# Kernel tuning notes

Hardware: AMD Instinct MI355X
Metric: run time of the kernel (lower is better)

Reference implementation:

```python
import jax, jax.numpy as jnp
import numpy as np

B, N, DIM = 16, 4096, 256
EXP = 4
COV_EPS = 1e-08


def setup_inputs() -> dict:
    key = jax.random.key(0)
    ks = jax.random.split(key, 9)
    s = 1.0 / np.sqrt(DIM)
    sh = 1.0 / np.sqrt(DIM * EXP)
    return {
        "x": jax.random.normal(ks[0], (B, N, DIM), dtype=jnp.float32),
        # IsoFFN: Linear(dim, 4*dim) -> GELU -> Linear(4*dim, dim) + residual (dropout inactive at eval)
        "W1": jax.random.uniform(ks[1], (DIM, DIM * EXP), minval=-s, maxval=s, dtype=jnp.float32),
        "b1": jnp.zeros((DIM * EXP,), jnp.float32),
        "W2": jax.random.uniform(ks[2], (DIM * EXP, DIM), minval=-sh, maxval=sh, dtype=jnp.float32),
        "b2": jnp.zeros((DIM,), jnp.float32),
        # eigenvalue head: Linear(dim, 3) + Softplus
        "Wval": jax.random.uniform(ks[3], (DIM, 3), minval=-s, maxval=s, dtype=jnp.float32),
        "bval": jnp.zeros((3,), jnp.float32),
        # eigenvector head: Linear(dim, 9)
        "Wvec": jax.random.uniform(ks[4], (DIM, 9), minval=-s, maxval=s, dtype=jnp.float32),
        "bvec": jnp.zeros((9,), jnp.float32),
    }


def reference(x, W1, b1, W2, b2, Wval, bval, Wvec, bvec):
    b, n, c = x.shape
    # IsoFFN (eval mode: dropout = identity), residual connection
    h = x + jax.nn.gelu(x @ W1 + b1) @ W2 + b2
    # eigenvalue head -> positive eigenvalues -> diagonal [B*N, 3, 3]
    eigvals = jax.nn.softplus(h @ Wval + bval).reshape(b * n, 3)
    L = jnp.zeros((b * n, 3, 3), h.dtype).at[:, jnp.arange(3), jnp.arange(3)].set(eigvals)
    # eigenvector head -> batched tiny QR to orthonormalize
    V = (h @ Wvec + bvec).reshape(b * n, 3, 3)
    Q, _ = jnp.linalg.qr(V)  # batched 3x3 QR
    # cov = Q L Q^T
    cov = jnp.einsum('bij,bjk,blk->bil', Q, L, Q).reshape(b, n, 3, 3)
    cov = (cov + jnp.swapaxes(cov, -2, -1)) * 0.5
    cov = cov + COV_EPS * jnp.eye(3, dtype=cov.dtype)
    return cov
```

## Files before the change

kernel.cpp:

```cpp
#include <hip/hip_runtime.h>
#include <cstdint>
#include <cstddef>

#define TOKENS   65536
#define KDIM     256
#define HIDDEN   1024
#define BM       128
#define HC       32
#define NCHUNK   32
#define NTHREADS 512
#define NBLOCKS  (TOKENS / BM)

#define W2OFF  32768
#define GOFF   65536
#define ACCOFF 81920
#define B1OFF  98304
#define LDS_BYTES 131072

using f16x8 = __attribute__((ext_vector_type(8))) _Float16;
using f16x4 = __attribute__((ext_vector_type(4))) _Float16;
using f32x4 = __attribute__((ext_vector_type(4))) float;
using u32x4 = __attribute__((ext_vector_type(4))) uint32_t;

__device__ __align__(16) _Float16 g_W1h[NCHUNK * HC * KDIM];
__device__ __align__(16) _Float16 g_W1l[NCHUNK * HC * KDIM];
__device__ __align__(16) _Float16 g_W2h[NCHUNK * KDIM * HC];
__device__ __align__(16) _Float16 g_W2l[NCHUNK * KDIM * HC];
__device__ __align__(16) _Float16 g_Whh[16 * KDIM];
__device__ __align__(16) _Float16 g_Whl[16 * KDIM];

__global__ __launch_bounds__(256) void prep_kernel(
    const float* __restrict__ W1, const float* __restrict__ W2,
    const float* __restrict__ Wval, const float* __restrict__ Wvec) {
  const int tid = blockIdx.x * 256 + threadIdx.x;
  if (tid < 32768) {
    const int c = tid >> 10, n = (tid >> 5) & 31, gd = tid & 31;
    const int g = gd ^ (n & 7);
    const int hid = c * 32 + n;
    f16x8 hv, lv;
#pragma unroll
    for (int j = 0; j < 8; ++j) {
      const float wv = W1[(g * 8 + j) * HIDDEN + hid];
      const _Float16 hi = (_Float16)wv;
      hv[j] = hi;
      lv[j] = (_Float16)(wv - (float)hi);
    }
    const int dst = c * 8192 + n * 256 + gd * 8;
    *(f16x8*)(g_W1h + dst) = hv;
    *(f16x8*)(g_W1l + dst) = lv;
  } else if (tid < 65536) {
    const int t = tid - 32768;
    const int c = t >> 10, n = (t >> 2) & 255, gd = t & 3;
    const int g = gd ^ ((n >> 1) & 3);
    f16x8 hv, lv;
#pragma unroll
    for (int j = 0; j < 8; ++j) {
      const float wv = W2[(c * 32 + g * 8 + j) * KDIM + n];
      const _Float16 hi = (_Float16)wv;
      hv[j] = hi;
      lv[j] = (_Float16)(wv - (float)hi);
    }
    const int dst = c * 8192 + n * 32 + gd * 8;
    *(f16x8*)(g_W2h + dst) = hv;
    *(f16x8*)(g_W2l + dst) = lv;
  } else if (tid < 65536 + 4096) {
    const int e = tid - 65536;
    const int j16 = e >> 8, k = e & 255;
    float wv = 0.f;
    if (j16 < 3) wv = Wval[k * 3 + j16];
    else if (j16 < 12) wv = Wvec[k * 9 + (j16 - 3)];
    const _Float16 hi = (_Float16)wv;
    g_Whh[e] = hi;
    g_Whl[e] = (_Float16)(wv - (float)hi);
  }
}

__device__ __forceinline__ void stage_W1(char* smem, int c, int w, int lane) {
  const char* base = (w < 4) ? (const char*)g_W1h : (const char*)g_W1l;
  const char* s = base + (size_t)c * 16384 + (size_t)(w & 3) * 4096 + (size_t)lane * 16;
  char* d = smem + ((w < 4) ? 0 : 16384) + (w & 3) * 4096;
#pragma unroll
  for (int i = 0; i < 4; ++i) {
    __builtin_amdgcn_global_load_lds(
        (__attribute__((address_space(1))) void*)(void*)(s + i * 1024),
        (__attribute__((address_space(3))) void*)(d + i * 1024), 16, 0, 0);
  }
}
__device__ __forceinline__ void stage_W2(char* smem, int c, int w, int lane) {
  const char* base = (w < 4) ? (const char*)g_W2h : (const char*)g_W2l;
  const char* s = base + (size_t)c * 16384 + (size_t)(w & 3) * 4096 + (size_t)lane * 16;
  char* d = smem + W2OFF + ((w < 4) ? 0 : 16384) + (w & 3) * 4096;
#pragma unroll
  for (int i = 0; i < 4; ++i) {
    __builtin_amdgcn_global_load_lds(
        (__attribute__((address_space(1))) void*)(void*)(s + i * 1024),
        (__attribute__((address_space(3))) void*)(d + i * 1024), 16, 0, 0);
  }
}

__device__ __forceinline__ f16x8 unpack_half(const u32x4 a, const u32x4 b, uint32_t sel) {
  u32x4 r;
  r[0] = __builtin_amdgcn_perm(a[1], a[0], sel);
  r[1] = __builtin_amdgcn_perm(a[3], a[2], sel);
  r[2] = __builtin_amdgcn_perm(b[1], b[0], sel);
  r[3] = __builtin_amdgcn_perm(b[3], b[2], sel);
  return __builtin_bit_cast(f16x8, r);
}

#define MFMA16(a, b, c) __builtin_amdgcn_mfma_f32_16x16x32_f16((a), (b), (c), 0, 0, 0)

__global__ __launch_bounds__(NTHREADS, 2) void fused_kernel(
    const float* __restrict__ x, const float* __restrict__ b1,
    const float* __restrict__ b2, const float* __restrict__ bval,
    const float* __restrict__ bvec, float* __restrict__ out) {
  extern __shared__ char smem[];
  const int tid  = threadIdx.x;
  const int lane = tid & 63;
  const int w    = tid >> 6;
  const int wm   = w & 3;
  const int wp   = w >> 2;
  const int l15  = lane & 15;
  const int lg   = lane >> 4;
  const int64_t R = (int64_t)blockIdx.x * BM;

  {
    const float* xg = x + R * KDIM;
#pragma unroll
    for (int i = 0; i < 16; ++i) {
      const int fidx = tid + NTHREADS * i;
      const int row  = fidx >> 6;
      const int f4   = fidx & 63;
      const float4 v = *(const float4*)(xg + row * KDIM + f4 * 4);
      const _Float16 h0 = (_Float16)v.x, h1 = (_Float16)v.y,
                     h2 = (_Float16)v.z, h3 = (_Float16)v.w;
      f16x4 hv = {h0, h1, h2, h3};
      f16x4 lv = {(_Float16)(v.x - (float)h0), (_Float16)(v.y - (float)h1),
                  (_Float16)(v.z - (float)h2), (_Float16)(v.w - (float)h3)};
      const uint32_t off = (uint32_t)(row * 512) +
                           (((uint32_t)(f4 * 8)) ^ ((row & 7) << 4));
      *(f16x4*)(smem + off)         = hv;
      *(f16x4*)(smem + 65536 + off) = lv;
    }
  }
  __syncthreads();

  f16x8 xa[2][8];
  {
    const char* xplane = smem + wp * 65536;
#pragma unroll
    for (int mt = 0; mt < 2; ++mt) {
      const int row = wm * 32 + mt * 16 + l15;
      const uint32_t rbase = row * 512;
      const uint32_t swz = (row & 7) << 4;
#pragma unroll
      for (int ks = 0; ks < 8; ++ks) {
        const uint32_t off = rbase + (((uint32_t)((ks * 32 + lg * 8) * 2)) ^ swz);
        xa[mt][ks] = *(const f16x8*)(xplane + off);
      }
    }
  }
  __syncthreads();

  {
    float* b1l = (float*)(smem + B1OFF);
    b1l[tid]       = b1[tid];
    b1l[tid + 512] = b1[tid + 512];
  }
  stage_W1(smem, 0, w, lane);
  __syncthreads();

  const f32x4 z4 = {0.f, 0.f, 0.f, 0.f};
  f32x4 acc2[2][8];
#pragma unroll
  for (int mt = 0; mt < 2; ++mt)
#pragma unroll
    for (int nt = 0; nt < 8; ++nt) acc2[mt][nt] = z4;

#pragma unroll 1
  for (int t = 0; t < NCHUNK; ++t) {
    stage_W2(smem, t, w, lane);

    f32x4 accG[8] = {z4, z4, z4, z4, z4, z4, z4, z4};
    {
      const uint32_t swz   = (uint32_t)((l15 & 7) << 4);
      const uint32_t base0 = (uint32_t)(l15 * 512);
      const uint32_t base1 = (uint32_t)((16 + l15) * 512);
      if (wp == 0) {
#pragma unroll
        for (int ks = 0; ks < 8; ++ks) {
          const uint32_t off = ((uint32_t)(ks * 64 + lg * 16)) ^ swz;
          const f16x8 bh0 = *(const f16x8*)(smem + base0 + off);
          const f16x8 bh1 = *(const f16x8*)(smem + base1 + off);
          const f16x8 bl0 = *(const f16x8*)(smem + 16384 + base0 + off);
          const f16x8 bl1 = *(const f16x8*)(smem + 16384 + base1 + off);
          accG[0] = MFMA16(xa[0][ks], bh0, accG[0]);
          accG[1] = MFMA16(xa[1][ks], bh0, accG[1]);
          accG[2] = MFMA16(xa[0][ks], bh1, accG[2]);
          accG[3] = MFMA16(xa[1][ks], bh1, accG[3]);
          accG[4] = MFMA16(xa[0][ks], bl0, accG[4]);
          accG[5] = MFMA16(xa[1][ks], bl0, accG[5]);
          accG[6] = MFMA16(xa[0][ks], bl1, accG[6]);
          accG[7] = MFMA16(xa[1][ks], bl1, accG[7]);
        }
      } else {
#pragma unroll
        for (int ks = 0; ks < 8; ++ks) {
          const uint32_t off = ((uint32_t)(ks * 64 + lg * 16)) ^ swz;
          const f16x8 bh0 = *(const f16x8*)(smem + base0 + off);
          const f16x8 bh1 = *(const f16x8*)(smem + base1 + off);
          accG[0] = MFMA16(xa[0][ks], bh0, accG[0]);
          accG[1] = MFMA16(xa[1][ks], bh0, accG[1]);
          accG[2] = MFMA16(xa[0][ks], bh1, accG[2]);
          accG[3] = MFMA16(xa[1][ks], bh1, accG[3]);
        }
#pragma unroll
        for (int nt = 0; nt < 2; ++nt) {
#pragma unroll
          for (int mt = 0; mt < 2; ++mt) {
#pragma unroll
            for (int r = 0; r < 4; ++r) {
              const int row = wm * 32 + mt * 16 + lg * 4 + r;
              const int col = nt * 16 + l15;
              const uint32_t off = (uint32_t)(ACCOFF + row * 128) +
                                   (((uint32_t)(col * 4)) ^ ((row & 7) << 4));
              *(float*)(smem + off) = accG[nt * 2 + mt][r];
            }
          }
        }
      }
    }
    asm volatile("s_waitcnt lgkmcnt(0)" ::: "memory");
    __builtin_amdgcn_s_barrier();
    __builtin_amdgcn_sched_barrier(0);

    if (t < NCHUNK - 1) stage_W1(smem, t + 1, w, lane);

    if (wp == 0) {
      constexpr float C2 = -1.5957691216057308f;
      constexpr float A2 = -0.071355071222456f;
#pragma unroll
      for (int nt = 0; nt < 2; ++nt) {
        const float bv = ((const float*)(smem + B1OFF))[t * 32 + nt * 16 + l15];
#pragma unroll
        for (int mt = 0; mt < 2; ++mt) {
#pragma unroll
          for (int r = 0; r < 4; ++r) {
            const int row = wm * 32 + mt * 16 + lg * 4 + r;
            const int col = nt * 16 + l15;
            const uint32_t soff = (((uint32_t)(col * 4)) ^ ((row & 7) << 4));
            const float c = *(const float*)(smem + ACCOFF + row * 128 + soff);
            const float v  = accG[nt * 2 + mt][r] + accG[4 + nt * 2 + mt][r] + c + bv;
            const float v2 = v * v;
            const float tE = v * __builtin_fmaf(v2, A2, C2);
            const float e  = __expf(tE);
            const float gv = __fdividef(v, 1.f + e);
            const _Float16 gh = (_Float16)gv;
            const _Float16 gl = (_Float16)(gv - (float)gh);
            const uint32_t pk = (uint32_t)__builtin_bit_cast(unsigned short, gh) |
                                ((uint32_t)__builtin_bit_cast(unsigned short, gl) << 16);
            *(uint32_t*)(smem + GOFF + row * 128 + soff) = pk;
          }
        }
      }
    }
    asm volatile("s_waitcnt lgkmcnt(0)" ::: "memory");
    if (t == NCHUNK - 1) { asm volatile("s_waitcnt vmcnt(0)" ::: "memory"); }
    else                 { asm volatile("s_waitcnt vmcnt(4)" ::: "memory"); }
    __builtin_amdgcn_s_barrier();
    __builtin_amdgcn_sched_barrier(0);

    {
      f16x8 ah[2], al[2];
#pragma unroll
      for (int mt = 0; mt < 2; ++mt) {
        const int row = wm * 32 + mt * 16 + l15;
        const uint32_t sw = (uint32_t)((row & 7) << 4);
        const uint32_t base = (uint32_t)(GOFF + row * 128);
        const u32x4 w0 = *(const u32x4*)(smem + base + (((uint32_t)(lg * 32)) ^ sw));
        const u32x4 w1v = *(const u32x4*)(smem + base + (((uint32_t)(lg * 32 + 16)) ^ sw));
        ah[mt] = unpack_half(w0, w1v, 0x05040100u);
        al[mt] = unpack_half(w0, w1v, 0x07060302u);
      }
#pragma unroll
      for (int nt = 0; nt < 8; ++nt) {
        const int n = wp * 128 + nt * 16 + l15;
        const uint32_t off = (uint32_t)(n * 64) +
                             (((uint32_t)(lg * 16)) ^ (((n >> 1) & 3) << 4));
        const f16x8 bh = *(const f16x8*)(smem + W2OFF + off);
        const f16x8 bl = *(const f16x8*)(smem + W2OFF + 16384 + off);
#pragma unroll
        for (int mt = 0; mt < 2; ++mt) {
          acc2[mt][nt] = MFMA16(ah[mt], bh, acc2[mt][nt]);
          acc2[mt][nt] = MFMA16(ah[mt], bl, acc2[mt][nt]);
          acc2[mt][nt] = MFMA16(al[mt], bh, acc2[mt][nt]);
        }
      }
    }
    asm volatile("s_waitcnt lgkmcnt(0)" ::: "memory");
    asm volatile("s_waitcnt vmcnt(0)" ::: "memory");
    __builtin_amdgcn_s_barrier();
    __builtin_amdgcn_sched_barrier(0);
  }
  __syncthreads();

  {
    const float* xg = x + R * KDIM;
#pragma unroll
    for (int nt = 0; nt < 8; ++nt) {
      const float bv = b2[wp * 128 + nt * 16 + l15];
#pragma unroll
      for (int mt = 0; mt < 2; ++mt) {
#pragma unroll
        for (int r = 0; r < 4; ++r) {
          const int row = wm * 32 + mt * 16 + lg * 4 + r;
          const int col = wp * 128 + nt * 16 + l15;
          const float h = acc2[mt][nt][r] + xg[row * KDIM + col] + bv;
          acc2[mt][nt][r] = h;
          const uint32_t off = (uint32_t)(row * 512) +
                               (((uint32_t)(col * 2)) ^ ((row & 7) << 4));
          *(_Float16*)(smem + off) = (_Float16)h;
        }
      }
    }
  }
  __syncthreads();

  f32x4 hacc = z4;
  const int hrow = wm * 32 + wp * 16 + l15;
  const uint32_t hbase = hrow * 512;
  const uint32_t hswz  = (hrow & 7) << 4;
#pragma unroll
  for (int ks = 0; ks < 8; ++ks) {
    const uint32_t off = hbase + (((uint32_t)((ks * 32 + lg * 8) * 2)) ^ hswz);
    const f16x8 af  = *(const f16x8*)(smem + off);
    const f16x8 bhf = *(const f16x8*)(g_Whh + l15 * 256 + ks * 32 + lg * 8);
    const f16x8 blf = *(const f16x8*)(g_Whl + l15 * 256 + ks * 32 + lg * 8);
    hacc = MFMA16(af, bhf, hacc);
    hacc = MFMA16(af, blf, hacc);
  }
  __syncthreads();

#pragma unroll
  for (int nt = 0; nt < 8; ++nt) {
#pragma unroll
    for (int mt = 0; mt < 2; ++mt) {
#pragma unroll
      for (int r = 0; r < 4; ++r) {
        const int row = wm * 32 + mt * 16 + lg * 4 + r;
        const int col = wp * 128 + nt * 16 + l15;
        const float h = acc2[mt][nt][r];
        const _Float16 hh = (_Float16)h;
        const uint32_t off = (uint32_t)(row * 512) +
                             (((uint32_t)(col * 2)) ^ ((row & 7) << 4));
        *(_Float16*)(smem + off) = (_Float16)(h - (float)hh);
      }
    }
  }
  __syncthreads();

#pragma unroll
  for (int ks = 0; ks < 8; ++ks) {
    const uint32_t off = hbase + (((uint32_t)((ks * 32 + lg * 8) * 2)) ^ hswz);
    const f16x8 af  = *(const f16x8*)(smem + off);
    const f16x8 bhf = *(const f16x8*)(g_Whh + l15 * 256 + ks * 32 + lg * 8);
    hacc = MFMA16(af, bhf, hacc);
  }
  const float hb = (l15 < 3) ? bval[l15] : ((l15 < 12) ? bvec[l15 - 3] : 0.f);
#pragma unroll
  for (int r = 0; r < 4; ++r) hacc[r] += hb;

  float* hstg = (float*)(smem + 65536);
#pragma unroll
  for (int r = 0; r < 4; ++r) {
    const int row = wm * 32 + wp * 16 + lg * 4 + r;
    hstg[row * 16 + l15] = hacc[r];
  }
  if (lane < 16) {
    const int row = wm * 32 + wp * 16 + lane;
    const float* hs = hstg + row * 16;
    float sp[3];
#pragma unroll
    for (int i = 0; i < 3; ++i) {
      const float s = hs[i];
      sp[i] = fmaxf(s, 0.f) + log1pf(__expf(-fabsf(s)));
    }
    const float a0 = hs[3], a1 = hs[6], a2 = hs[9];
    const float b0 = hs[4], bc1 = hs[7], bc2 = hs[10];
    const float na = a0 * a0 + a1 * a1 + a2 * a2;
    const float ia = 1.f / sqrtf(fmaxf(na, 1e-30f));
    const float q00 = a0 * ia, q01 = a1 * ia, q02 = a2 * ia;
    const float d  = q00 * b0 + q01 * bc1 + q02 * bc2;
    const float u0 = b0 - d * q00, u1 = bc1 - d * q01, u2 = bc2 - d * q02;
    const float nu = u0 * u0 + u1 * u1 + u2 * u2;
    const float iu = 1.f / sqrtf(fmaxf(nu, 1e-30f));
    const float q10 = u0 * iu, q11 = u1 * iu, q12 = u2 * iu;
    const float q20 = q01 * q12 - q02 * q11;
    const float q21 = q02 * q10 - q00 * q12;
    const float q22 = q00 * q11 - q01 * q10;
    const float c00 = sp[0]*q00*q00 + sp[1]*q10*q10 + sp[2]*q20*q20 + 1e-8f;
    const float c11 = sp[0]*q01*q01 + sp[1]*q11*q11 + sp[2]*q21*q21 + 1e-8f;
    const float c22 = sp[0]*q02*q02 + sp[1]*q12*q12 + sp[2]*q22*q22 + 1e-8f;
    const float c01 = sp[0]*q00*q01 + sp[1]*q10*q11 + sp[2]*q20*q21;
    const float c02 = sp[0]*q00*q02 + sp[1]*q10*q12 + sp[2]*q20*q22;
    const float c12 = sp[0]*q01*q02 + sp[1]*q11*q12 + sp[2]*q21*q22;
    float* o = out + (size_t)(R + row) * 9;
    o[0] = c00; o[1] = c01; o[2] = c02;
    o[3] = c01; o[4] = c11; o[5] = c12;
    o[6] = c02; o[7] = c12; o[8] = c22;
  }
}

extern "C" void kernel_launch(void* const* d_in, const int* in_sizes, int n_in,
                              void* d_out, int out_size, void* d_ws, size_t ws_size,
                              hipStream_t stream) {
  const float* x    = (const float*)d_in[0];
  const float* W1   = (const float*)d_in[1];
  const float* b1   = (const float*)d_in[2];
  const float* W2   = (const float*)d_in[3];
  const float* b2   = (const float*)d_in[4];
  const float* Wval = (const float*)d_in[5];
  const float* bval = (const float*)d_in[6];
  const float* Wvec = (const float*)d_in[7];
  const float* bvec = (const float*)d_in[8];
  float* out = (float*)d_out;
  (void)in_sizes; (void)n_in; (void)out_size; (void)d_ws; (void)ws_size;

  hipFuncSetAttribute((const void*)fused_kernel,
                      hipFuncAttributeMaxDynamicSharedMemorySize, LDS_BYTES);

  prep_kernel<<<272, 256, 0, stream>>>(W1, W2, Wval, Wvec);
  fused_kernel<<<NBLOCKS, NTHREADS, LDS_BYTES, stream>>>(x, b1, b2, bval, bvec, out);
}
```

Before: 319.5 us.

## Halve token tile to 64 rows and raise occupancy to four blocks per CU

Shrinks the per-block token tile from 128 to 64 rows, cutting per-wave accumulators and x fragments in half and shrinking LDS so four 512-thread blocks can fit per CU instead of two. The cross-plane partial accumulator exchange for the GELU input is now stored as fp16 instead of fp32. The head epilogue is restricted to the first four waves since only 64 rows remain. In exchange, each W1/W2 chunk staged into LDS is reused across half as many tokens, doubling weight traffic per token. The fp16 partial sum also loses some precision.

```diff
diff --git a/kernel.cpp b/kernel.cpp
--- a/kernel.cpp
+++ b/kernel.cpp
@@ -5,7 +5,7 @@
 #define TOKENS   65536
 #define KDIM     256
 #define HIDDEN   1024
-#define BM       128
+#define BM       64
 #define HC       32
 #define NCHUNK   32
 #define NTHREADS 512
@@ -13,9 +13,9 @@
 
 #define W2OFF  32768
 #define GOFF   65536
-#define ACCOFF 81920
-#define B1OFF  98304
-#define LDS_BYTES 131072
+#define ACCOFF 73728
+#define B1OFF  77824
+#define LDS_BYTES 81920
 
 using f16x8 = __attribute__((ext_vector_type(8))) _Float16;
 using f16x4 = __attribute__((ext_vector_type(4))) _Float16;
@@ -109,7 +109,7 @@
 
 #define MFMA16(a, b, c) __builtin_amdgcn_mfma_f32_16x16x32_f16((a), (b), (c), 0, 0, 0)
 
-__global__ __launch_bounds__(NTHREADS, 2) void fused_kernel(
+__global__ __launch_bounds__(NTHREADS, 4) void fused_kernel(
     const float* __restrict__ x, const float* __restrict__ b1,
     const float* __restrict__ b2, const float* __restrict__ bval,
     const float* __restrict__ bvec, float* __restrict__ out) {
@@ -126,7 +126,7 @@
   {
     const float* xg = x + R * KDIM;
 #pragma unroll
-    for (int i = 0; i < 16; ++i) {
+    for (int i = 0; i < 8; ++i) {
       const int fidx = tid + NTHREADS * i;
       const int row  = fidx >> 6;
       const int f4   = fidx & 63;
@@ -139,24 +139,21 @@
       const uint32_t off = (uint32_t)(row * 512) +
                            (((uint32_t)(f4 * 8)) ^ ((row & 7) << 4));
       *(f16x4*)(smem + off)         = hv;
-      *(f16x4*)(smem + 65536 + off) = lv;
-    }
-  }
-  __syncthreads();
-
-  f16x8 xa[2][8];
+      *(f16x4*)(smem + 32768 + off) = lv;
+    }
+  }
+  __syncthreads();
+
+  f16x8 xa[8];
   {
-    const char* xplane = smem + wp * 65536;
-#pragma unroll
-    for (int mt = 0; mt < 2; ++mt) {
-      const int row = wm * 32 + mt * 16 + l15;
-      const uint32_t rbase = row * 512;
-      const uint32_t swz = (row & 7) << 4;
-#pragma unroll
-      for (int ks = 0; ks < 8; ++ks) {
-        const uint32_t off = rbase + (((uint32_t)((ks * 32 + lg * 8) * 2)) ^ swz);
-        xa[mt][ks] = *(const f16x8*)(xplane + off);
-      }
+    const char* xplane = smem + wp * 32768;
+    const int row = wm * 16 + l15;
+    const uint32_t rbase = row * 512;
+    const uint32_t swz = (row & 7) << 4;
+#pragma unroll
+    for (int ks = 0; ks < 8; ++ks) {
+      const uint32_t off = rbase + (((uint32_t)((ks * 32 + lg * 8) * 2)) ^ swz);
+      xa[ks] = *(const f16x8*)(xplane + off);
     }
   }
   __syncthreads();
@@ -170,17 +167,15 @@
   __syncthreads();
 
   const f32x4 z4 = {0.f, 0.f, 0.f, 0.f};
-  f32x4 acc2[2][8];
-#pragma unroll
-  for (int mt = 0; mt < 2; ++mt)
-#pragma unroll
-    for (int nt = 0; nt < 8; ++nt) acc2[mt][nt] = z4;
+  f32x4 acc2[8];
+#pragma unroll
+  for (int nt = 0; nt < 8; ++nt) acc2[nt] = z4;
 
 #pragma unroll 1
   for (int t = 0; t < NCHUNK; ++t) {
     stage_W2(smem, t, w, lane);
 
-    f32x4 accG[8] = {z4, z4, z4, z4, z4, z4, z4, z4};
+    f32x4 accA[2] = {z4, z4}, accB[2] = {z4, z4};
     {
       const uint32_t swz   = (uint32_t)((l15 & 7) << 4);
       const uint32_t base0 = (uint32_t)(l15 * 512);
@@ -193,14 +188,10 @@
           const f16x8 bh1 = *(const f16x8*)(smem + base1 + off);
           const f16x8 bl0 = *(const f16x8*)(smem + 16384 + base0 + off);
           const f16x8 bl1 = *(const f16x8*)(smem + 16384 + base1 + off);
-          accG[0] = MFMA16(xa[0][ks], bh0, accG[0]);
-          accG[1] = MFMA16(xa[1][ks], bh0, accG[1]);
-          accG[2] = MFMA16(xa[0][ks], bh1, accG[2]);
-          accG[3] = MFMA16(xa[1][ks], bh1, accG[3]);
-          accG[4] = MFMA16(xa[0][ks], bl0, accG[4]);
-          accG[5] = MFMA16(xa[1][ks], bl0, accG[5]);
-          accG[6] = MFMA16(xa[0][ks], bl1, accG[6]);
-          accG[7] = MFMA16(xa[1][ks], bl1, accG[7]);
+          accA[0] = MFMA16(xa[ks], bh0, accA[0]);
+          accA[1] = MFMA16(xa[ks], bh1, accA[1]);
+          accB[0] = MFMA16(xa[ks], bl0, accB[0]);
+          accB[1] = MFMA16(xa[ks], bl1, accB[1]);
         }
       } else {
 #pragma unroll
@@ -208,23 +199,18 @@
           const uint32_t off = ((uint32_t)(ks * 64 + lg * 16)) ^ swz;
           const f16x8 bh0 = *(const f16x8*)(smem + base0 + off);
           const f16x8 bh1 = *(const f16x8*)(smem + base1 + off);
-          accG[0] = MFMA16(xa[0][ks], bh0, accG[0]);
-          accG[1] = MFMA16(xa[1][ks], bh0, accG[1]);
-          accG[2] = MFMA16(xa[0][ks], bh1, accG[2]);
-          accG[3] = MFMA16(xa[1][ks], bh1, accG[3]);
+          accA[0] = MFMA16(xa[ks], bh0, accA[0]);
+          accA[1] = MFMA16(xa[ks], bh1, accA[1]);
         }
 #pragma unroll
         for (int nt = 0; nt < 2; ++nt) {
 #pragma unroll
-          for (int mt = 0; mt < 2; ++mt) {
-#pragma unroll
-            for (int r = 0; r < 4; ++r) {
-              const int row = wm * 32 + mt * 16 + lg * 4 + r;
-              const int col = nt * 16 + l15;
-              const uint32_t off = (uint32_t)(ACCOFF + row * 128) +
-                                   (((uint32_t)(col * 4)) ^ ((row & 7) << 4));
-              *(float*)(smem + off) = accG[nt * 2 + mt][r];
-            }
+          for (int r = 0; r < 4; ++r) {
+            const int row = wm * 16 + lg * 4 + r;
+            const int col = nt * 16 + l15;
+            const uint32_t off = (uint32_t)(ACCOFF + row * 64) +
+                                 (((uint32_t)(col * 2)) ^ ((row & 3) << 4));
+            *(_Float16*)(smem + off) = (_Float16)accA[nt][r];
           }
         }
       }
@@ -242,24 +228,24 @@
       for (int nt = 0; nt < 2; ++nt) {
         const float bv = ((const float*)(smem + B1OFF))[t * 32 + nt * 16 + l15];
 #pragma unroll
-        for (int mt = 0; mt < 2; ++mt) {
-#pragma unroll
-          for (int r = 0; r < 4; ++r) {
-            const int row = wm * 32 + mt * 16 + lg * 4 + r;
-            const int col = nt * 16 + l15;
-            const uint32_t soff = (((uint32_t)(col * 4)) ^ ((row & 7) << 4));
-            const float c = *(const float*)(smem + ACCOFF + row * 128 + soff);
-            const float v  = accG[nt * 2 + mt][r] + accG[4 + nt * 2 + mt][r] + c + bv;
-            const float v2 = v * v;
-            const float tE = v * __builtin_fmaf(v2, A2, C2);
-            const float e  = __expf(tE);
-            const float gv = __fdividef(v, 1.f + e);
-            const _Float16 gh = (_Float16)gv;
-            const _Float16 gl = (_Float16)(gv - (float)gh);
-            const uint32_t pk = (uint32_t)__builtin_bit_cast(unsigned short, gh) |
-                                ((uint32_t)__builtin_bit_cast(unsigned short, gl) << 16);
-            *(uint32_t*)(smem + GOFF + row * 128 + soff) = pk;
-          }
+        for (int r = 0; r < 4; ++r) {
+          const int row = wm * 16 + lg * 4 + r;
+          const int col = nt * 16 + l15;
+          const uint32_t coff = (uint32_t)(ACCOFF + row * 64) +
+                                (((uint32_t)(col * 2)) ^ ((row & 3) << 4));
+          const float c = (float)(*(const _Float16*)(smem + coff));
+          const float v  = accA[nt][r] + accB[nt][r] + c + bv;
+          const float v2 = v * v;
+          const float tE = v * __builtin_fmaf(v2, A2, C2);
+          const float e  = __expf(tE);
+          const float gv = __fdividef(v, 1.f + e);
+          const _Float16 gh = (_Float16)gv;
+          const _Float16 gl = (_Float16)(gv - (float)gh);
+          const uint32_t pk = (uint32_t)__builtin_bit_cast(unsigned short, gh) |
+                              ((uint32_t)__builtin_bit_cast(unsigned short, gl) << 16);
+          const uint32_t goff = (uint32_t)(GOFF + row * 128) +
+                                (((uint32_t)(col * 4)) ^ ((row & 7) << 4));
+          *(uint32_t*)(smem + goff) = pk;
         }
       }
     }
@@ -270,16 +256,15 @@
     __builtin_amdgcn_sched_barrier(0);
 
     {
-      f16x8 ah[2], al[2];
-#pragma unroll
-      for (int mt = 0; mt < 2; ++mt) {
-        const int row = wm * 32 + mt * 16 + l15;
+      f16x8 ah, al;
+      {
+        const int row = wm * 16 + l15;
         const uint32_t sw = (uint32_t)((row & 7) << 4);
         const uint32_t base = (uint32_t)(GOFF + row * 128);
         const u32x4 w0 = *(const u32x4*)(smem + base + (((uint32_t)(lg * 32)) ^ sw));
         const u32x4 w1v = *(const u32x4*)(smem + base + (((uint32_t)(lg * 32 + 16)) ^ sw));
-        ah[mt] = unpack_half(w0, w1v, 0x05040100u);
-        al[mt] = unpack_half(w0, w1v, 0x07060302u);
+        ah = unpack_half(w0, w1v, 0x05040100u);
+        al = unpack_half(w0, w1v, 0x07060302u);
       }
 #pragma unroll
       for (int nt = 0; nt < 8; ++nt) {
@@ -288,12 +273,9 @@
                              (((uint32_t)(lg * 16)) ^ (((n >> 1) & 3) << 4));
         const f16x8 bh = *(const f16x8*)(smem + W2OFF + off);
         const f16x8 bl = *(const f16x8*)(smem + W2OFF + 16384 + off);
-#pragma unroll
-        for (int mt = 0; mt < 2; ++mt) {
-          acc2[mt][nt] = MFMA16(ah[mt], bh, acc2[mt][nt]);
-          acc2[mt][nt] = MFMA16(ah[mt], bl, acc2[mt][nt]);
-          acc2[mt][nt] = MFMA16(al[mt], bh, acc2[mt][nt]);
-        }
+        acc2[nt] = MFMA16(ah, bh, acc2[nt]);
+        acc2[nt] = MFMA16(ah, bl, acc2[nt]);
+        acc2[nt] = MFMA16(al, bh, acc2[nt]);
       }
     }
     asm volatile("s_waitcnt lgkmcnt(0)" ::: "memory");
@@ -309,104 +291,105 @@
     for (int nt = 0; nt < 8; ++nt) {
       const float bv = b2[wp * 128 + nt * 16 + l15];
 #pragma unroll
-      for (int mt = 0; mt < 2; ++mt) {
-#pragma unroll
-        for (int r = 0; r < 4; ++r) {
-          const int row = wm * 32 + mt * 16 + lg * 4 + r;
-          const int col = wp * 128 + nt * 16 + l15;
-          const float h = acc2[mt][nt][r] + xg[row * KDIM + col] + bv;
-          acc2[mt][nt][r] = h;
-          const uint32_t off = (uint32_t)(row * 512) +
-                               (((uint32_t)(col * 2)) ^ ((row & 7) << 4));
-          *(_Float16*)(smem + off) = (_Float16)h;
-        }
+      for (int r = 0; r < 4; ++r) {
+        const int row = wm * 16 + lg * 4 + r;
+        const int col = wp * 128 + nt * 16 + l15;
+        const float h = acc2[nt][r] + xg[row * KDIM + col] + bv;
+        acc2[nt][r] = h;
+        const uint32_t off = (uint32_t)(row * 512) +
+                             (((uint32_t)(col * 2)) ^ ((row & 7) << 4));
+        *(_Float16*)(smem + off) = (_Float16)h;
       }
     }
   }
   __syncthreads();
 
   f32x4 hacc = z4;
-  const int hrow = wm * 32 + wp * 16 + l15;
+  const int hrow = w * 16 + l15;
   const uint32_t hbase = hrow * 512;
   const uint32_t hswz  = (hrow & 7) << 4;
-#pragma unroll
-  for (int ks = 0; ks < 8; ++ks) {
-    const uint32_t off = hbase + (((uint32_t)((ks * 32 + lg * 8) * 2)) ^ hswz);
-    const f16x8 af  = *(const f16x8*)(smem + off);
-    const f16x8 bhf = *(const f16x8*)(g_Whh + l15 * 256 + ks * 32 + lg * 8);
-    const f16x8 blf = *(const f16x8*)(g_Whl + l15 * 256 + ks * 32 + lg * 8);
-    hacc = MFMA16(af, bhf, hacc);
-    hacc = MFMA16(af, blf, hacc);
+  if (w < 4) {
+#pragma unroll
+    for (int ks = 0; ks < 8; ++ks) {
+      const uint32_t off = hbase + (((uint32_t)((ks * 32 + lg * 8) * 2)) ^ hswz);
+      const f16x8 af  = *(const f16x8*)(smem + off);
+      const f16x8 bhf = *(const f16x8*)(g_Whh + l15 * 256 + ks * 32 + lg * 8);
+      const f16x8 blf = *(const f16x8*)(g_Whl + l15 * 256 + ks * 32 + lg * 8);
+      hacc = MFMA16(af, bhf, hacc);
+      hacc = MFMA16(af, blf, hacc);
+    }
   }
   __syncthreads();
 
 #pragma unroll
   for (int nt = 0; nt < 8; ++nt) {
 #pragma unroll
-    for (int mt = 0; mt < 2; ++mt) {
-#pragma unroll
-      for (int r = 0; r < 4; ++r) {
-        const int row = wm * 32 + mt * 16 + lg * 4 + r;
-        const int col = wp * 128 + nt * 16 + l15;
-        const float h = acc2[mt][nt][r];
-        const _Float16 hh = (_Float16)h;
-        const uint32_t off = (uint32_t)(row * 512) +
-                             (((uint32_t)(col * 2)) ^ ((row & 7) << 4));
-        *(_Float16*)(smem + off) = (_Float16)(h - (float)hh);
-      }
-    }
-  }
-  __syncthreads();
-
-#pragma unroll
-  for (int ks = 0; ks < 8; ++ks) {
-    const uint32_t off = hbase + (((uint32_t)((ks * 32 + lg * 8) * 2)) ^ hswz);
-    const f16x8 af  = *(const f16x8*)(smem + off);
-    const f16x8 bhf = *(const f16x8*)(g_Whh + l15 * 256 + ks * 32 + lg * 8);
-    hacc = MFMA16(af, bhf, hacc);
-  }
-  const float hb = (l15 < 3) ? bval[l15] : ((l15 < 12) ? bvec[l15 - 3] : 0.f);
-#pragma unroll
-  for (int r = 0; r < 4; ++r) hacc[r] += hb;
-
-  float* hstg = (float*)(smem + 65536);
-#pragma unroll
-  for (int r = 0; r < 4; ++r) {
-    const int row = wm * 32 + wp * 16 + lg * 4 + r;
-    hstg[row * 16 + l15] = hacc[r];
-  }
-  if (lane < 16) {
-    const int row = wm * 32 + wp * 16 + lane;
-    const float* hs = hstg + row * 16;
-    float sp[3];
-#pragma unroll
-    for (int i = 0; i < 3; ++i) {
-      const float s = hs[i];
-      sp[i] = fmaxf(s, 0.f) + log1pf(__expf(-fabsf(s)));
-    }
-    const float a0 = hs[3], a1 = hs[6], a2 = hs[9];
-    const float b0 = hs[4], bc1 = hs[7], bc2 = hs[10];
-    const float na = a0 * a0 + a1 * a1 + a2 * a2;
-    const float ia = 1.f / sqrtf(fmaxf(na, 1e-30f));
-    const float q00 = a0 * ia, q01 = a1 * ia, q02 = a2 * ia;
-    const float d  = q00 * b0 + q01 * bc1 + q02 * bc2;
-    const float u0 = b0 - d * q00, u1 = bc1 - d * q01, u2 = bc2 - d * q02;
-    const float nu = u0 * u0 + u1 * u1 + u2 * u2;
-    const float iu = 1.f / sqrtf(fmaxf(nu, 1e-30f));
-    const float q10 = u0 * iu, q11 = u1 * iu, q12 = u2 * iu;
-    const float q20 = q01 * q12 - q02 * q11;
-    const float q21 = q02 * q10 - q00 * q12;
-    const float q22 = q00 * q11 - q01 * q10;
-    const float c00 = sp[0]*q00*q00 + sp[1]*q10*q10 + sp[2]*q20*q20 + 1e-8f;
-    const float c11 = sp[0]*q01*q01 + sp[1]*q11*q11 + sp[2]*q21*q21 + 1e-8f;
-    const float c22 = sp[0]*q02*q02 + sp[1]*q12*q12 + sp[2]*q22*q22 + 1e-8f;
-    const float c01 = sp[0]*q00*q01 + sp[1]*q10*q11 + sp[2]*q20*q21;
-    const float c02 = sp[0]*q00*q02 + sp[1]*q10*q12 + sp[2]*q20*q22;
-    const float c12 = sp[0]*q01*q02 + sp[1]*q11*q12 + sp[2]*q21*q22;
-    float* o = out + (size_t)(R + row) * 9;
-    o[0] = c00; o[1] = c01; o[2] = c02;
-    o[3] = c01; o[4] = c11; o[5] = c12;
-    o[6] = c02; o[7] = c12; o[8] = c22;
+    for (int r = 0; r < 4; ++r) {
+      const int row = wm * 16 + lg * 4 + r;
+      const int col = wp * 128 + nt * 16 + l15;
+      const float h = acc2[nt][r];
+      const _Float16 hh = (_Float16)h;
+      const uint32_t off = (uint32_t)(row * 512) +
+                           (((uint32_t)(col * 2)) ^ ((row & 7) << 4));
+      *(_Float16*)(smem + off) = (_Float16)(h - (float)hh);
+    }
+  }
+  __syncthreads();
+
+  if (w < 4) {
+#pragma unroll
+    for (int ks = 0; ks < 8; ++ks) {
+      const uint32_t off = hbase + (((uint32_t)((ks * 32 + lg * 8) * 2)) ^ hswz);
+      const f16x8 af  = *(const f16x8*)(smem + off);
+      const f16x8 bhf = *(const f16x8*)(g_Whh + l15 * 256 + ks * 32 + lg * 8);
+      hacc = MFMA16(af, bhf, hacc);
+    }
+    const float hb = (l15 < 3) ? bval[l15] : ((l15 < 12) ? bvec[l15 - 3] : 0.f);
+#pragma unroll
+    for (int r = 0; r < 4; ++r) hacc[r] += hb;
+  }
+  __syncthreads();
+
+  float* hstg = (float*)(smem + 32768);
+  if (w < 4) {
+#pragma unroll
+    for (int r = 0; r < 4; ++r) {
+      const int row = w * 16 + lg * 4 + r;
+      hstg[row * 16 + l15] = hacc[r];
+    }
+    if (lane < 16) {
+      const int row = w * 16 + lane;
+      const float* hs = hstg + row * 16;
+      float sp[3];
+#pragma unroll
+      for (int i = 0; i < 3; ++i) {
+        const float s = hs[i];
+        sp[i] = fmaxf(s, 0.f) + log1pf(__expf(-fabsf(s)));
+      }
+      const float a0 = hs[3], a1 = hs[6], a2 = hs[9];
+      const float b0 = hs[4], bc1 = hs[7], bc2 = hs[10];
+      const float na = a0 * a0 + a1 * a1 + a2 * a2;
+      const float ia = 1.f / sqrtf(fmaxf(na, 1e-30f));
+      const float q00 = a0 * ia, q01 = a1 * ia, q02 = a2 * ia;
+      const float d  = q00 * b0 + q01 * bc1 + q02 * bc2;
+      const float u0 = b0 - d * q00, u1 = bc1 - d * q01, u2 = bc2 - d * q02;
+      const float nu = u0 * u0 + u1 * u1 + u2 * u2;
+      const float iu = 1.f / sqrtf(fmaxf(nu, 1e-30f));
+      const float q10 = u0 * iu, q11 = u1 * iu, q12 = u2 * iu;
+      const float q20 = q01 * q12 - q02 * q11;
+      const float q21 = q02 * q10 - q00 * q12;
+      const float q22 = q00 * q11 - q01 * q10;
+      const float c00 = sp[0]*q00*q00 + sp[1]*q10*q10 + sp[2]*q20*q20 + 1e-8f;
+      const float c11 = sp[0]*q01*q01 + sp[1]*q11*q11 + sp[2]*q21*q21 + 1e-8f;
+      const float c22 = sp[0]*q02*q02 + sp[1]*q12*q12 + sp[2]*q22*q22 + 1e-8f;
+      const float c01 = sp[0]*q00*q01 + sp[1]*q10*q11 + sp[2]*q20*q21;
+      const float c02 = sp[0]*q00*q02 + sp[1]*q10*q12 + sp[2]*q20*q22;
+      const float c12 = sp[0]*q01*q02 + sp[1]*q11*q12 + sp[2]*q21*q22;
+      float* o = out + (size_t)(R + row) * 9;
+      o[0] = c00; o[1] = c01; o[2] = c02;
+      o[3] = c01; o[4] = c11; o[5] = c12;
+      o[6] = c02; o[7] = c12; o[8] = c22;
+    }
   }
 }
 
```

After: 319.4 us. Within noise of the previous version (-0.1%).

## Double hidden chunk width to 64 and reuse G buffer for partial accumulators

Applied to the files above, without the earlier changes.

Widens each hidden-dimension chunk from 32 to 64 columns, which halves the number of loop iterations and their barriers, and resizes the W1/W2 staging layouts and swizzles to match. The cross-wave partial accumulator now goes through the G region as fp16 in place of a separate fp32 area, and the b1 bias is prefetched into registers instead of being staged in LDS. The cost is more LDS (163840 bytes), which may reduce occupancy below two blocks per CU, plus extra precision loss from storing the partial sum in fp16.

```diff
diff --git a/kernel.cpp b/kernel.cpp
--- a/kernel.cpp
+++ b/kernel.cpp
@@ -6,16 +6,14 @@
 #define KDIM     256
 #define HIDDEN   1024
 #define BM       128
-#define HC       32
-#define NCHUNK   32
+#define HC       64
+#define NCHUNK   16
 #define NTHREADS 512
 #define NBLOCKS  (TOKENS / BM)
 
-#define W2OFF  32768
-#define GOFF   65536
-#define ACCOFF 81920
-#define B1OFF  98304
-#define LDS_BYTES 131072
+#define W2OFF  65536
+#define GOFF   131072
+#define LDS_BYTES 163840
 
 using f16x8 = __attribute__((ext_vector_type(8))) _Float16;
 using f16x4 = __attribute__((ext_vector_type(4))) _Float16;
@@ -34,9 +32,9 @@
     const float* __restrict__ Wval, const float* __restrict__ Wvec) {
   const int tid = blockIdx.x * 256 + threadIdx.x;
   if (tid < 32768) {
-    const int c = tid >> 10, n = (tid >> 5) & 31, gd = tid & 31;
+    const int c = tid >> 11, n = (tid >> 5) & 63, gd = tid & 31;
     const int g = gd ^ (n & 7);
-    const int hid = c * 32 + n;
+    const int hid = c * 64 + n;
     f16x8 hv, lv;
 #pragma unroll
     for (int j = 0; j < 8; ++j) {
@@ -45,22 +43,22 @@
       hv[j] = hi;
       lv[j] = (_Float16)(wv - (float)hi);
     }
-    const int dst = c * 8192 + n * 256 + gd * 8;
+    const int dst = c * 16384 + n * 256 + gd * 8;
     *(f16x8*)(g_W1h + dst) = hv;
     *(f16x8*)(g_W1l + dst) = lv;
   } else if (tid < 65536) {
     const int t = tid - 32768;
-    const int c = t >> 10, n = (t >> 2) & 255, gd = t & 3;
-    const int g = gd ^ ((n >> 1) & 3);
+    const int c = t >> 11, n = (t >> 3) & 255, gd = t & 7;
+    const int g = gd ^ (n & 7);
     f16x8 hv, lv;
 #pragma unroll
     for (int j = 0; j < 8; ++j) {
-      const float wv = W2[(c * 32 + g * 8 + j) * KDIM + n];
+      const float wv = W2[(c * 64 + g * 8 + j) * KDIM + n];
       const _Float16 hi = (_Float16)wv;
       hv[j] = hi;
       lv[j] = (_Float16)(wv - (float)hi);
     }
-    const int dst = c * 8192 + n * 32 + gd * 8;
+    const int dst = c * 16384 + n * 64 + gd * 8;
     *(f16x8*)(g_W2h + dst) = hv;
     *(f16x8*)(g_W2l + dst) = lv;
   } else if (tid < 65536 + 4096) {
@@ -77,10 +75,10 @@
 
 __device__ __forceinline__ void stage_W1(char* smem, int c, int w, int lane) {
   const char* base = (w < 4) ? (const char*)g_W1h : (const char*)g_W1l;
-  const char* s = base + (size_t)c * 16384 + (size_t)(w & 3) * 4096 + (size_t)lane * 16;
-  char* d = smem + ((w < 4) ? 0 : 16384) + (w & 3) * 4096;
-#pragma unroll
-  for (int i = 0; i < 4; ++i) {
+  const char* s = base + (size_t)c * 32768 + (size_t)(w & 3) * 8192 + (size_t)lane * 16;
+  char* d = smem + ((w < 4) ? 0 : 32768) + (w & 3) * 8192;
+#pragma unroll
+  for (int i = 0; i < 8; ++i) {
     __builtin_amdgcn_global_load_lds(
         (__attribute__((address_space(1))) void*)(void*)(s + i * 1024),
         (__attribute__((address_space(3))) void*)(d + i * 1024), 16, 0, 0);
@@ -88,10 +86,10 @@
 }
 __device__ __forceinline__ void stage_W2(char* smem, int c, int w, int lane) {
   const char* base = (w < 4) ? (const char*)g_W2h : (const char*)g_W2l;
-  const char* s = base + (size_t)c * 16384 + (size_t)(w & 3) * 4096 + (size_t)lane * 16;
-  char* d = smem + W2OFF + ((w < 4) ? 0 : 16384) + (w & 3) * 4096;
-#pragma unroll
-  for (int i = 0; i < 4; ++i) {
+  const char* s = base + (size_t)c * 32768 + (size_t)(w & 3) * 8192 + (size_t)lane * 16;
+  char* d = smem + W2OFF + ((w < 4) ? 0 : 32768) + (w & 3) * 8192;
+#pragma unroll
+  for (int i = 0; i < 8; ++i) {
     __builtin_amdgcn_global_load_lds(
         (__attribute__((address_space(1))) void*)(void*)(s + i * 1024),
         (__attribute__((address_space(3))) void*)(d + i * 1024), 16, 0, 0);
@@ -161,11 +159,9 @@
   }
   __syncthreads();
 
-  {
-    float* b1l = (float*)(smem + B1OFF);
-    b1l[tid]       = b1[tid];
-    b1l[tid + 512] = b1[tid + 512];
-  }
+  float b_cur[4];
+#pragma unroll
+  for (int nt = 0; nt < 4; ++nt) b_cur[nt] = b1[nt * 16 + l15];
   stage_W1(smem, 0, w, lane);
   __syncthreads();
 
@@ -180,50 +176,51 @@
   for (int t = 0; t < NCHUNK; ++t) {
     stage_W2(smem, t, w, lane);
 
-    f32x4 accG[8] = {z4, z4, z4, z4, z4, z4, z4, z4};
+    f32x4 accA[2][4], accB[2][4];
+#pragma unroll
+    for (int mt = 0; mt < 2; ++mt)
+#pragma unroll
+      for (int nt = 0; nt < 4; ++nt) { accA[mt][nt] = z4; accB[mt][nt] = z4; }
     {
-      const uint32_t swz   = (uint32_t)((l15 & 7) << 4);
-      const uint32_t base0 = (uint32_t)(l15 * 512);
-      const uint32_t base1 = (uint32_t)((16 + l15) * 512);
+      const uint32_t swz = (uint32_t)((l15 & 7) << 4);
       if (wp == 0) {
 #pragma unroll
         for (int ks = 0; ks < 8; ++ks) {
-          const uint32_t off = ((uint32_t)(ks * 64 + lg * 16)) ^ swz;
-          const f16x8 bh0 = *(const f16x8*)(smem + base0 + off);
-          const f16x8 bh1 = *(const f16x8*)(smem + base1 + off);
-          const f16x8 bl0 = *(const f16x8*)(smem + 16384 + base0 + off);
-          const f16x8 bl1 = *(const f16x8*)(smem + 16384 + base1 + off);
-          accG[0] = MFMA16(xa[0][ks], bh0, accG[0]);
-          accG[1] = MFMA16(xa[1][ks], bh0, accG[1]);
-          accG[2] = MFMA16(xa[0][ks], bh1, accG[2]);
-          accG[3] = MFMA16(xa[1][ks], bh1, accG[3]);
-          accG[4] = MFMA16(xa[0][ks], bl0, accG[4]);
-          accG[5] = MFMA16(xa[1][ks], bl0, accG[5]);
-          accG[6] = MFMA16(xa[0][ks], bl1, accG[6]);
-          accG[7] = MFMA16(xa[1][ks], bl1, accG[7]);
+          const uint32_t ko = (uint32_t)(ks * 64 + lg * 16);
+#pragma unroll
+          for (int nt = 0; nt < 4; ++nt) {
+            const uint32_t off = (uint32_t)((nt * 16 + l15) * 512) + (ko ^ swz);
+            const f16x8 bh = *(const f16x8*)(smem + off);
+            const f16x8 bl = *(const f16x8*)(smem + 32768 + off);
+            accA[0][nt] = MFMA16(xa[0][ks], bh, accA[0][nt]);
+            accA[1][nt] = MFMA16(xa[1][ks], bh, accA[1][nt]);
+            accB[0][nt] = MFMA16(xa[0][ks], bl, accB[0][nt]);
+            accB[1][nt] = MFMA16(xa[1][ks], bl, accB[1][nt]);
+          }
         }
       } else {
 #pragma unroll
         for (int ks = 0; ks < 8; ++ks) {
-          const uint32_t off = ((uint32_t)(ks * 64 + lg * 16)) ^ swz;
-          const f16x8 bh0 = *(const f16x8*)(smem + base0 + off);
-          const f16x8 bh1 = *(const f16x8*)(smem + base1 + off);
-          accG[0] = MFMA16(xa[0][ks], bh0, accG[0]);
-          accG[1] = MFMA16(xa[1][ks], bh0, accG[1]);
-          accG[2] = MFMA16(xa[0][ks], bh1, accG[2]);
-          accG[3] = MFMA16(xa[1][ks], bh1, accG[3]);
-        }
-#pragma unroll
-        for (int nt = 0; nt < 2; ++nt) {
-#pragma unroll
-          for (int mt = 0; mt < 2; ++mt) {
+          const uint32_t ko = (uint32_t)(ks * 64 + lg * 16);
+#pragma unroll
+          for (int nt = 0; nt < 4; ++nt) {
+            const uint32_t off = (uint32_t)((nt * 16 + l15) * 512) + (ko ^ swz);
+            const f16x8 bh = *(const f16x8*)(smem + off);
+            accA[0][nt] = MFMA16(xa[0][ks], bh, accA[0][nt]);
+            accA[1][nt] = MFMA16(xa[1][ks], bh, accA[1][nt]);
+          }
+        }
+#pragma unroll
+        for (int mt = 0; mt < 2; ++mt) {
+#pragma unroll
+          for (int nt = 0; nt < 4; ++nt) {
 #pragma unroll
             for (int r = 0; r < 4; ++r) {
               const int row = wm * 32 + mt * 16 + lg * 4 + r;
               const int col = nt * 16 + l15;
-              const uint32_t off = (uint32_t)(ACCOFF + row * 128) +
+              const uint32_t off = (uint32_t)(GOFF + row * 256) +
                                    (((uint32_t)(col * 4)) ^ ((row & 7) << 4));
-              *(float*)(smem + off) = accG[nt * 2 + mt][r];
+              *(_Float16*)(smem + off) = (_Float16)accA[mt][nt][r];
             }
           }
         }
@@ -233,23 +230,29 @@
     __builtin_amdgcn_s_barrier();
     __builtin_amdgcn_sched_barrier(0);
 
-    if (t < NCHUNK - 1) stage_W1(smem, t + 1, w, lane);
+    float b_nxt[4];
+    if (t < NCHUNK - 1) {
+#pragma unroll
+      for (int nt = 0; nt < 4; ++nt)
+        b_nxt[nt] = b1[(t + 1) * 64 + nt * 16 + l15];
+      stage_W1(smem, t + 1, w, lane);
+    }
 
     if (wp == 0) {
       constexpr float C2 = -1.5957691216057308f;
       constexpr float A2 = -0.071355071222456f;
 #pragma unroll
-      for (int nt = 0; nt < 2; ++nt) {
-        const float bv = ((const float*)(smem + B1OFF))[t * 32 + nt * 16 + l15];
-#pragma unroll
-        for (int mt = 0; mt < 2; ++mt) {
+      for (int mt = 0; mt < 2; ++mt) {
+#pragma unroll
+        for (int nt = 0; nt < 4; ++nt) {
 #pragma unroll
           for (int r = 0; r < 4; ++r) {
             const int row = wm * 32 + mt * 16 + lg * 4 + r;
             const int col = nt * 16 + l15;
-            const uint32_t soff = (((uint32_t)(col * 4)) ^ ((row & 7) << 4));
-            const float c = *(const float*)(smem + ACCOFF + row * 128 + soff);
-            const float v  = accG[nt * 2 + mt][r] + accG[4 + nt * 2 + mt][r] + c + bv;
+            const uint32_t off = (uint32_t)(GOFF + row * 256) +
+                                 (((uint32_t)(col * 4)) ^ ((row & 7) << 4));
+            const float c = (float)(*(const _Float16*)(smem + off));
+            const float v  = accA[mt][nt][r] + accB[mt][nt][r] + c + b_cur[nt];
             const float v2 = v * v;
             const float tE = v * __builtin_fmaf(v2, A2, C2);
             const float e  = __expf(tE);
@@ -258,36 +261,41 @@
             const _Float16 gl = (_Float16)(gv - (float)gh);
             const uint32_t pk = (uint32_t)__builtin_bit_cast(unsigned short, gh) |
                                 ((uint32_t)__builtin_bit_cast(unsigned short, gl) << 16);
-            *(uint32_t*)(smem + GOFF + row * 128 + soff) = pk;
+            *(uint32_t*)(smem + off) = pk;
           }
         }
       }
+    }
+    if (t < NCHUNK - 1) {
+#pragma unroll
+      for (int nt = 0; nt < 4; ++nt) b_cur[nt] = b_nxt[nt];
     }
     asm volatile("s_waitcnt lgkmcnt(0)" ::: "memory");
     if (t == NCHUNK - 1) { asm volatile("s_waitcnt vmcnt(0)" ::: "memory"); }
-    else                 { asm volatile("s_waitcnt vmcnt(4)" ::: "memory"); }
+    else                 { asm volatile("s_waitcnt vmcnt(12)" ::: "memory"); }
     __builtin_amdgcn_s_barrier();
     __builtin_amdgcn_sched_barrier(0);
 
-    {
+#pragma unroll
+    for (int ks2 = 0; ks2 < 2; ++ks2) {
       f16x8 ah[2], al[2];
 #pragma unroll
       for (int mt = 0; mt < 2; ++mt) {
         const int row = wm * 32 + mt * 16 + l15;
         const uint32_t sw = (uint32_t)((row & 7) << 4);
-        const uint32_t base = (uint32_t)(GOFF + row * 128);
-        const u32x4 w0 = *(const u32x4*)(smem + base + (((uint32_t)(lg * 32)) ^ sw));
-        const u32x4 w1v = *(const u32x4*)(smem + base + (((uint32_t)(lg * 32 + 16)) ^ sw));
+        const uint32_t base = (uint32_t)(GOFF + row * 256);
+        const u32x4 w0 = *(const u32x4*)(smem + base + (((uint32_t)(ks2 * 128 + lg * 32)) ^ sw));
+        const u32x4 w1v = *(const u32x4*)(smem + base + (((uint32_t)(ks2 * 128 + lg * 32 + 16)) ^ sw));
         ah[mt] = unpack_half(w0, w1v, 0x05040100u);
         al[mt] = unpack_half(w0, w1v, 0x07060302u);
       }
 #pragma unroll
       for (int nt = 0; nt < 8; ++nt) {
         const int n = wp * 128 + nt * 16 + l15;
-        const uint32_t off = (uint32_t)(n * 64) +
-                             (((uint32_t)(lg * 16)) ^ (((n >> 1) & 3) << 4));
+        const uint32_t off = (uint32_t)(n * 128) +
+                             (((uint32_t)(ks2 * 64 + lg * 16)) ^ ((n & 7) << 4));
         const f16x8 bh = *(const f16x8*)(smem + W2OFF + off);
-        const f16x8 bl = *(const f16x8*)(smem + W2OFF + 16384 + off);
+        const f16x8 bl = *(const f16x8*)(smem + W2OFF + 32768 + off);
 #pragma unroll
         for (int mt = 0; mt < 2; ++mt) {
           acc2[mt][nt] = MFMA16(ah[mt], bh, acc2[mt][nt]);
```

After: 794.0 us. 148% more time.
